# Optimization experiments

Hardware: AMD Instinct MI355X
Metric: run time of the kernel (lower is better)

The kernel has to match this reference:

```python
import jax, jax.numpy as jnp
import numpy as np

# Reconstructed from DAT's DAttentionBaseline with the wrapper's config:
# q_size=(14,14), n_heads=12, n_head_channels=64, n_groups=8, stride=1,
# offset_range_factor=1.0, use_pe=False (so log_cpb/rpe unused), no_off=False,
# ksize=3, dropout=0 (eval). Followed by the wrapper's Linear out-projection.

H = W = 14
G = 8          # n_groups
NH = 12        # n_heads
OFF_RANGE_FACTOR = 1.0


def grid_sample_bilinear(img, grid):
    # img: [B, C, H, W]; grid: [B, Hg, Wg, 2] in (x, y) order, [-1, 1],
    # align_corners=True, padding_mode='zeros' (torch defaults used by DAT).
    B, C, Hi, Wi = img.shape
    gx = (grid[..., 0] + 1.0) * 0.5 * (Wi - 1)
    gy = (grid[..., 1] + 1.0) * 0.5 * (Hi - 1)
    x0 = jnp.floor(gx)
    y0 = jnp.floor(gy)
    x1 = x0 + 1.0
    y1 = y0 + 1.0
    wx1 = gx - x0
    wx0 = 1.0 - wx1
    wy1 = gy - y0
    wy0 = 1.0 - wy1
    flat = img.reshape(B, C, Hi * Wi)

    def tap(xi, yi, wgt):
        valid = (xi >= 0) & (xi <= Wi - 1) & (yi >= 0) & (yi <= Hi - 1)
        xi_c = jnp.clip(xi, 0, Wi - 1).astype(jnp.int32)
        yi_c = jnp.clip(yi, 0, Hi - 1).astype(jnp.int32)
        idx = (yi_c * Wi + xi_c).reshape(B, 1, -1)
        vals = jnp.take_along_axis(flat, idx, axis=2)  # [B, C, Hg*Wg]
        w = (wgt * valid.astype(img.dtype)).reshape(B, 1, -1)
        return vals * w

    out = (tap(x0, y0, wx0 * wy0) + tap(x1, y0, wx1 * wy0)
           + tap(x0, y1, wx0 * wy1) + tap(x1, y1, wx1 * wy1))
    return out  # [B, C, Hg*Wg]


def setup_inputs() -> dict:
    key = jax.random.key(0)
    ks = jax.random.split(key, 16)
    B, N, C = 128, 196, 768
    Cg = C // G  # 96
    s = 0.02
    return {
        "hidden_states": jax.random.normal(ks[0], (B, N, C), jnp.float32),
        "Wq": jax.random.normal(ks[1], (C, C), jnp.float32) * s,
        "bq": jnp.zeros((C,), jnp.float32),
        "off_dw_w": jax.random.normal(ks[2], (Cg, 1, 3, 3), jnp.float32) * s,
        "off_dw_b": jnp.zeros((Cg,), jnp.float32),
        "ln_w": jnp.ones((Cg,), jnp.float32),
        "ln_b": jnp.zeros((Cg,), jnp.float32),
        "off_pw_w": jax.random.normal(ks[3], (2, Cg), jnp.float32) * s,
        "Wk": jax.random.normal(ks[4], (C, C), jnp.float32) * s,
        "bk": jnp.zeros((C,), jnp.float32),
        "Wv": jax.random.normal(ks[5], (C, C), jnp.float32) * s,
        "bv": jnp.zeros((C,), jnp.float32),
        "Wproj": jax.random.normal(ks[6], (C, C), jnp.float32) * s,
        "bproj": jnp.zeros((C,), jnp.float32),
        "Wout": jax.random.normal(ks[7], (C, C), jnp.float32) * s,
        "bout": jnp.zeros((C,), jnp.float32),
    }


def reference(hidden_states, Wq, bq, off_dw_w, off_dw_b, ln_w, ln_b, off_pw_w,
              Wk, bk, Wv, bv, Wproj, bproj, Wout, bout):
    B, N, C = hidden_states.shape
    Cg = C // G
    nh, dh = NH, C // NH
    scale = dh ** -0.5
    dt = hidden_states.dtype

    x_im = hidden_states.reshape(B, H, W, C).transpose(0, 3, 1, 2)  # [B,C,H,W]

    # proj_q: 1x1 conv
    q_im = jnp.einsum('bchw,oc->bohw', x_im, Wq) + bq[None, :, None, None]
    q_off = q_im.reshape(B * G, Cg, H, W)

    # offset net: depthwise 3x3 conv -> LayerNorm(channels) -> GELU -> 1x1 (no bias)
    t = jax.lax.conv_general_dilated(
        q_off, off_dw_w, (1, 1), [(1, 1), (1, 1)],
        dimension_numbers=('NCHW', 'OIHW', 'NCHW'), feature_group_count=Cg)
    t = t + off_dw_b[None, :, None, None]
    mu = t.mean(axis=1, keepdims=True)
    var = ((t - mu) ** 2).mean(axis=1, keepdims=True)
    t = (t - mu) * jax.lax.rsqrt(var + 1e-5)
    t = t * ln_w[None, :, None, None] + ln_b[None, :, None, None]
    t = jax.nn.gelu(t, approximate=False)
    off = jnp.einsum('bchw,oc->bohw', t, off_pw_w)  # [B*G, 2(y,x), H, W]

    off_range = jnp.array([1.0 / (H - 1), 1.0 / (W - 1)], dt).reshape(1, 2, 1, 1)
    off = jnp.tanh(off) * off_range * OFF_RANGE_FACTOR
    off = off.transpose(0, 2, 3, 1)  # [B*G, H, W, 2] (y, x)

    ry = ((jnp.arange(H, dtype=dt) + 0.5) / H) * 2.0 - 1.0
    rx = ((jnp.arange(W, dtype=dt) + 0.5) / W) * 2.0 - 1.0
    ref = jnp.stack(jnp.meshgrid(ry, rx, indexing='ij'), axis=-1)  # [H,W,2]
    pos = off + ref[None]          # (y, x)
    grid = pos[..., ::-1]          # (x, y) for grid_sample

    x_g = x_im.reshape(B * G, Cg, H, W)
    n_sample = H * W
    x_s = grid_sample_bilinear(x_g, grid).reshape(B, C, n_sample)

    k = jnp.einsum('bcn,oc->bon', x_s, Wk) + bk[None, :, None]
    v = jnp.einsum('bcn,oc->bon', x_s, Wv) + bv[None, :, None]

    qh = q_im.reshape(B, nh, dh, N)
    kh = k.reshape(B, nh, dh, n_sample)
    vh = v.reshape(B, nh, dh, n_sample)

    attn = jax.nn.softmax(jnp.einsum('bhcm,bhcn->bhmn', qh, kh) * scale, axis=-1)
    out = jnp.einsum('bhmn,bhcn->bhcm', attn, vh).reshape(B, C, N)

    y = jnp.einsum('bcn,oc->bon', out, Wproj) + bproj[None, :, None]
    y = y.transpose(0, 2, 1)               # [B, N, C]
    y = y @ Wout.T + bout                  # wrapper's Linear out-projection
    return y, attn
```

## Files before the change

kernel.cpp:

```cpp
#include <hip/hip_runtime.h>
#include <math.h>

#define Bsz 128
#define Hh 14
#define Ww 14
#define Nn 196
#define Cc 768
#define Gg 8
#define CgC 96
#define NHh 12
#define Dh 64
#define ROWS (Bsz*Nn)

typedef _Float16 half8 __attribute__((ext_vector_type(8)));
typedef _Float16 half4 __attribute__((ext_vector_type(4)));
typedef float f32x4 __attribute__((ext_vector_type(4)));

typedef __attribute__((address_space(3))) void LDSv;
typedef __attribute__((address_space(1))) void GLBv;

__global__ __launch_bounds__(256) void cvt_w5(
    const float* __restrict__ w0, const float* __restrict__ w1,
    const float* __restrict__ w2, const float* __restrict__ w3,
    const float* __restrict__ w4, _Float16* __restrict__ dst)
{
  const int i = blockIdx.x * 256 + threadIdx.x;
  const int per = Cc * Cc / 8;
  if (i >= 5 * per) return;
  const int m = i / per, r = i - m * per;
  const float* s = (m == 0) ? w0 : (m == 1) ? w1 : (m == 2) ? w2 : (m == 3) ? w3 : w4;
  float4 a = *(const float4*)(s + (size_t)r * 8);
  float4 b = *(const float4*)(s + (size_t)r * 8 + 4);
  half8 h;
  h[0]=(_Float16)a.x; h[1]=(_Float16)a.y; h[2]=(_Float16)a.z; h[3]=(_Float16)a.w;
  h[4]=(_Float16)b.x; h[5]=(_Float16)b.y; h[6]=(_Float16)b.z; h[7]=(_Float16)b.w;
  *(half8*)(dst + (size_t)m * Cc * Cc + (size_t)r * 8) = h;
}

__global__ __launch_bounds__(256) void fuse_bias(
    const float* __restrict__ Wo, const float* __restrict__ bp,
    const float* __restrict__ bo, float* __restrict__ bf)
{
  __shared__ float red[256];
  const int o2 = blockIdx.x;
  const int tid = threadIdx.x;
  const float* wrow = Wo + (size_t)o2 * Cc;
  float s = 0.f;
  for (int o = tid; o < Cc; o += 256) s = fmaf(wrow[o], bp[o], s);
  red[tid] = s;
  __syncthreads();
  for (int st = 128; st > 0; st >>= 1) { if (tid < st) red[tid] += red[tid + st]; __syncthreads(); }
  if (tid == 0) bf[o2] = red[0] + bo[o2];
}

__global__ __launch_bounds__(256) void gemm_ww(
    const _Float16* __restrict__ Wo16, const _Float16* __restrict__ Wp16,
    _Float16* __restrict__ Wf)
{
  __shared__ __align__(16) _Float16 As[128 * 64];
  __shared__ __align__(16) _Float16 Bs[128 * 72];
  const int t = threadIdx.x;
  const int bid = blockIdx.x;
  const int colb = bid % 6, rowb = bid / 6;
  const int row0 = rowb * 128, col0 = colb * 128;
  const int lane = t & 63, w = t >> 6;
  const int wr = w >> 1, wc = w & 1;
  const int l15 = lane & 15, l4 = lane >> 4;
  const int srow = t >> 3;
  const int sg   = t & 7;

  f32x4 acc[4][4];
#pragma unroll
  for (int i = 0; i < 4; ++i)
#pragma unroll
    for (int j = 0; j < 4; ++j) acc[i][j] = (f32x4){0.f, 0.f, 0.f, 0.f};

  for (int kt = 0; kt < 12; ++kt) {
    const int k0 = kt * 64;
#pragma unroll
    for (int it = 0; it < 4; ++it) {
      const int r = it * 32 + srow;
      half8 ha = *(const half8*)(Wo16 + (size_t)(row0 + r) * Cc + k0 + sg * 8);
      *(half8*)&As[r * 64 + ((sg ^ (r & 7)) * 8)] = ha;
    }
    {
      const int og = t >> 4;
      const int cg = t & 15;
#pragma unroll
      for (int it = 0; it < 4; ++it) {
        const int o = it * 16 + og;
        half8 hv = *(const half8*)(Wp16 + (size_t)(k0 + o) * Cc + col0 + cg * 8);
#pragma unroll
        for (int e = 0; e < 8; ++e)
          Bs[(cg * 8 + e) * 72 + o] = hv[e];
      }
    }
    __syncthreads();
#pragma unroll
    for (int ks = 0; ks < 2; ++ks) {
      half8 af[4], bf[4];
#pragma unroll
      for (int mi = 0; mi < 4; ++mi) {
        const int r = wr * 64 + mi * 16 + l15;
        const int g = ks * 4 + l4;
        af[mi] = *(const half8*)&As[r * 64 + ((g ^ (r & 7)) * 8)];
      }
#pragma unroll
      for (int ni = 0; ni < 4; ++ni) {
        const int c = wc * 64 + ni * 16 + l15;
        bf[ni] = *(const half8*)&Bs[c * 72 + ks * 32 + l4 * 8];
      }
#pragma unroll
      for (int mi = 0; mi < 4; ++mi)
#pragma unroll
        for (int ni = 0; ni < 4; ++ni)
          acc[mi][ni] = __builtin_amdgcn_mfma_f32_16x16x32_f16(af[mi], bf[ni], acc[mi][ni], 0, 0, 0);
    }
    __syncthreads();
  }

#pragma unroll
  for (int ni = 0; ni < 4; ++ni) {
    const int col = col0 + wc * 64 + ni * 16 + l15;
#pragma unroll
    for (int mi = 0; mi < 4; ++mi) {
      f32x4 v = acc[mi][ni];
      const int rbase = row0 + wr * 64 + mi * 16 + l4 * 4;
#pragma unroll
      for (int r = 0; r < 4; ++r)
        Wf[(size_t)(rbase + r) * Cc + col] = (_Float16)v[r];
    }
  }
}

__global__ __launch_bounds__(256) void gemm_f32a(
    const float* __restrict__ A, const _Float16* __restrict__ W,
    const float* __restrict__ bias, _Float16* __restrict__ Cout)
{
  __shared__ __align__(16) _Float16 As[128 * 64];
  __shared__ __align__(16) _Float16 Bs[128 * 64];
  const int t = threadIdx.x;
  const int nwg = gridDim.x;
  int bid = blockIdx.x;
  bid = (bid & 7) * (nwg >> 3) + (bid >> 3);
  const int colb = bid % 6, rowb = bid / 6;
  const int row0 = rowb * 128, col0 = colb * 128;
  const int lane = t & 63, w = t >> 6;
  const int wr = w >> 1, wc = w & 1;
  const int l15 = lane & 15, l4 = lane >> 4;
  const int srow = t >> 3;
  const int sg   = t & 7;
  const int rl = lane >> 3;
  const int sl = lane & 7;

  f32x4 acc[4][4];
#pragma unroll
  for (int i = 0; i < 4; ++i)
#pragma unroll
    for (int j = 0; j < 4; ++j) acc[i][j] = (f32x4){0.f, 0.f, 0.f, 0.f};

  for (int kt = 0; kt < 12; ++kt) {
    const int k0 = kt * 64;
#pragma unroll
    for (int it = 0; it < 4; ++it) {
      const int rbase = it * 32 + w * 8;
      const int rw = rbase + rl;
      const int sa = sl ^ (rw & 7);
      __builtin_amdgcn_global_load_lds(
          (GLBv*)(W + (size_t)(col0 + rw) * Cc + k0 + sa * 8),
          (LDSv*)&Bs[rbase * 64], 16, 0, 0);
      const int r = it * 32 + srow;
      const float* ap = A + (size_t)(row0 + r) * Cc + k0 + sg * 8;
      float4 a0 = *(const float4*)ap;
      float4 a1 = *(const float4*)(ap + 4);
      half8 ha;
      ha[0]=(_Float16)a0.x; ha[1]=(_Float16)a0.y; ha[2]=(_Float16)a0.z; ha[3]=(_Float16)a0.w;
      ha[4]=(_Float16)a1.x; ha[5]=(_Float16)a1.y; ha[6]=(_Float16)a1.z; ha[7]=(_Float16)a1.w;
      *(half8*)&As[r * 64 + ((sg ^ (r & 7)) * 8)] = ha;
    }
    __syncthreads();
#pragma unroll
    for (int ks = 0; ks < 2; ++ks) {
      half8 af[4], bf[4];
#pragma unroll
      for (int mi = 0; mi < 4; ++mi) {
        const int r = wr * 64 + mi * 16 + l15;
        const int g = ks * 4 + l4;
        af[mi] = *(const half8*)&As[r * 64 + ((g ^ (r & 7)) * 8)];
      }
#pragma unroll
      for (int ni = 0; ni < 4; ++ni) {
        const int r = wc * 64 + ni * 16 + l15;
        const int g = ks * 4 + l4;
        bf[ni] = *(const half8*)&Bs[r * 64 + ((g ^ (r & 7)) * 8)];
      }
#pragma unroll
      for (int mi = 0; mi < 4; ++mi)
#pragma unroll
        for (int ni = 0; ni < 4; ++ni)
          acc[mi][ni] = __builtin_amdgcn_mfma_f32_16x16x32_f16(af[mi], bf[ni], acc[mi][ni], 0, 0, 0);
    }
    __syncthreads();
  }

#pragma unroll
  for (int ni = 0; ni < 4; ++ni) {
    const int col = col0 + wc * 64 + ni * 16 + l15;
    const float bcol = bias[col];
#pragma unroll
    for (int mi = 0; mi < 4; ++mi) {
      f32x4 v = acc[mi][ni];
      const int rbase = row0 + wr * 64 + mi * 16 + l4 * 4;
#pragma unroll
      for (int r = 0; r < 4; ++r)
        Cout[(size_t)(rbase + r) * Cc + col] = (_Float16)(v[r] + bcol);
    }
  }
}

template<int F16OUT>
__global__ __launch_bounds__(256) void gemm_h16(
    const _Float16* __restrict__ A, const _Float16* __restrict__ W,
    const float* __restrict__ bias, void* __restrict__ Cout)
{
  __shared__ __align__(16) _Float16 As[128 * 64];
  __shared__ __align__(16) _Float16 Bs[128 * 64];
  const int t = threadIdx.x;
  const int nwg = gridDim.x;
  int bid = blockIdx.x;
  bid = (bid & 7) * (nwg >> 3) + (bid >> 3);
  const int colb = bid % 6, rowb = bid / 6;
  const int row0 = rowb * 128, col0 = colb * 128;
  const int lane = t & 63, w = t >> 6;
  const int wr = w >> 1, wc = w & 1;
  const int l15 = lane & 15, l4 = lane >> 4;
  const int rl = lane >> 3;
  const int sl = lane & 7;

  f32x4 acc[4][4];
#pragma unroll
  for (int i = 0; i < 4; ++i)
#pragma unroll
    for (int j = 0; j < 4; ++j) acc[i][j] = (f32x4){0.f, 0.f, 0.f, 0.f};

  for (int kt = 0; kt < 12; ++kt) {
    const int k0 = kt * 64;
#pragma unroll
    for (int it = 0; it < 4; ++it) {
      const int rbase = it * 32 + w * 8;
      const int r = rbase + rl;
      const int sa = sl ^ (r & 7);
      __builtin_amdgcn_global_load_lds(
          (GLBv*)(A + (size_t)(row0 + r) * Cc + k0 + sa * 8),
          (LDSv*)&As[rbase * 64], 16, 0, 0);
      __builtin_amdgcn_global_load_lds(
          (GLBv*)(W + (size_t)(col0 + r) * Cc + k0 + sa * 8),
          (LDSv*)&Bs[rbase * 64], 16, 0, 0);
    }
    __syncthreads();
#pragma unroll
    for (int ks = 0; ks < 2; ++ks) {
      half8 af[4], bf[4];
#pragma unroll
      for (int mi = 0; mi < 4; ++mi) {
        const int r = wr * 64 + mi * 16 + l15;
        const int g = ks * 4 + l4;
        af[mi] = *(const half8*)&As[r * 64 + ((g ^ (r & 7)) * 8)];
      }
#pragma unroll
      for (int ni = 0; ni < 4; ++ni) {
        const int r = wc * 64 + ni * 16 + l15;
        const int g = ks * 4 + l4;
        bf[ni] = *(const half8*)&Bs[r * 64 + ((g ^ (r & 7)) * 8)];
      }
#pragma unroll
      for (int mi = 0; mi < 4; ++mi)
#pragma unroll
        for (int ni = 0; ni < 4; ++ni)
          acc[mi][ni] = __builtin_amdgcn_mfma_f32_16x16x32_f16(af[mi], bf[ni], acc[mi][ni], 0, 0, 0);
    }
    __syncthreads();
  }

#pragma unroll
  for (int ni = 0; ni < 4; ++ni) {
    const int col = col0 + wc * 64 + ni * 16 + l15;
    const float bcol = bias[col];
#pragma unroll
    for (int mi = 0; mi < 4; ++mi) {
      f32x4 v = acc[mi][ni];
      const int rbase = row0 + wr * 64 + mi * 16 + l4 * 4;
#pragma unroll
      for (int r = 0; r < 4; ++r) {
        if (F16OUT) {
          ((_Float16*)Cout)[(size_t)(rbase + r) * Cc + col] = (_Float16)(v[r] + bcol);
        } else {
          ((float*)Cout)[(size_t)(rbase + r) * Cc + col] = v[r] + bcol;
        }
      }
    }
  }
}

__global__ __launch_bounds__(256) void gemm_h16_kv(
    const _Float16* __restrict__ A, const _Float16* __restrict__ Wkv,
    const float* __restrict__ bk, const float* __restrict__ bv,
    _Float16* __restrict__ K16, _Float16* __restrict__ V16)
{
  __shared__ __align__(16) _Float16 As[128 * 64];
  __shared__ __align__(16) _Float16 Bs[128 * 64];
  const int t = threadIdx.x;
  const int nwg = gridDim.x;
  int bid = blockIdx.x;
  bid = (bid & 7) * (nwg >> 3) + (bid >> 3);
  const int colb = bid % 12, rowb = bid / 12;
  const int row0 = rowb * 128, col0 = colb * 128;
  const int lane = t & 63, w = t >> 6;
  const int wr = w >> 1, wc = w & 1;
  const int l15 = lane & 15, l4 = lane >> 4;
  const int rl = lane >> 3;
  const int sl = lane & 7;

  _Float16* Cout = (colb < 6) ? K16 : V16;
  const float* bias = (colb < 6) ? bk : bv;
  const int cadj = (colb < 6) ? 0 : Cc;

  f32x4 acc[4][4];
#pragma unroll
  for (int i = 0; i < 4; ++i)
#pragma unroll
    for (int j = 0; j < 4; ++j) acc[i][j] = (f32x4){0.f, 0.f, 0.f, 0.f};

  for (int kt = 0; kt < 12; ++kt) {
    const int k0 = kt * 64;
#pragma unroll
    for (int it = 0; it < 4; ++it) {
      const int rbase = it * 32 + w * 8;
      const int r = rbase + rl;
      const int sa = sl ^ (r & 7);
      __builtin_amdgcn_global_load_lds(
          (GLBv*)(A + (size_t)(row0 + r) * Cc + k0 + sa * 8),
          (LDSv*)&As[rbase * 64], 16, 0, 0);
      __builtin_amdgcn_global_load_lds(
          (GLBv*)(Wkv + (size_t)(col0 + r) * Cc + k0 + sa * 8),
          (LDSv*)&Bs[rbase * 64], 16, 0, 0);
    }
    __syncthreads();
#pragma unroll
    for (int ks = 0; ks < 2; ++ks) {
      half8 af[4], bf[4];
#pragma unroll
      for (int mi = 0; mi < 4; ++mi) {
        const int r = wr * 64 + mi * 16 + l15;
        const int g = ks * 4 + l4;
        af[mi] = *(const half8*)&As[r * 64 + ((g ^ (r & 7)) * 8)];
      }
#pragma unroll
      for (int ni = 0; ni < 4; ++ni) {
        const int r = wc * 64 + ni * 16 + l15;
        const int g = ks * 4 + l4;
        bf[ni] = *(const half8*)&Bs[r * 64 + ((g ^ (r & 7)) * 8)];
      }
#pragma unroll
      for (int mi = 0; mi < 4; ++mi)
#pragma unroll
        for (int ni = 0; ni < 4; ++ni)
          acc[mi][ni] = __builtin_amdgcn_mfma_f32_16x16x32_f16(af[mi], bf[ni], acc[mi][ni], 0, 0, 0);
    }
    __syncthreads();
  }

#pragma unroll
  for (int ni = 0; ni < 4; ++ni) {
    const int col = col0 + wc * 64 + ni * 16 + l15;
    const float bcol = bias[col - cadj];
#pragma unroll
    for (int mi = 0; mi < 4; ++mi) {
      f32x4 v = acc[mi][ni];
      const int rbase = row0 + wr * 64 + mi * 16 + l4 * 4;
#pragma unroll
      for (int r = 0; r < 4; ++r)
        Cout[(size_t)(rbase + r) * Cc + (col - cadj)] = (_Float16)(v[r] + bcol);
    }
  }
}

__global__ __launch_bounds__(512, 4) void offset_sample(
    const _Float16* __restrict__ Q16, const float* __restrict__ hidden,
    const float* __restrict__ dw_w, const float* __restrict__ dw_b,
    const float* __restrict__ ln_w, const float* __restrict__ ln_b,
    const float* __restrict__ pw_w, _Float16* __restrict__ XS)
{
  __shared__ float Qs[8 * Ww * CgC];
  const int tid = threadIdx.x;
  const int g    = blockIdx.x & 7;
  const int half = blockIdx.x >> 3;
  const int b = blockIdx.y;
  const int cl = tid & 31;
  const int grp = tid >> 5;
  const int hbase = half ? 6 : 0;

  const size_t base = (size_t)b * Nn * Cc + g * CgC;
  for (int i = tid; i < 8 * Ww * 12; i += 512) {
    const int n = i / 12, j = i - n * 12;
    const int gn = hbase * Ww + n;
    half8 hv = *(const half8*)(Q16 + base + (size_t)gn * Cc + j * 8);
#pragma unroll
    for (int e = 0; e < 8; ++e) Qs[n * CgC + j * 8 + e] = (float)hv[e];
  }

  float wdw[3][9], bdw[3], wln[3], bln[3], wp0[3], wp1[3];
#pragma unroll
  for (int k = 0; k < 3; ++k) {
    const int c = cl + k * 32;
#pragma unroll
    for (int t9 = 0; t9 < 9; ++t9) wdw[k][t9] = dw_w[c * 9 + t9];
    bdw[k] = dw_b[c];
    wln[k] = ln_w[c];
    bln[k] = ln_b[c];
    wp0[k] = pw_w[c];
    wp1[k] = pw_w[CgC + c];
  }
  __syncthreads();

  const float* hb0 = hidden + base;
  const int nsites = 7 * Ww;

  for (int s0 = 0; s0 < nsites; s0 += 16) {
    const int slcl = s0 + grp;
    if (slcl < nsites) {
      const int site = half * nsites + slcl;
      const int h = site / Ww, w = site % Ww;

      float t[3];
#pragma unroll
      for (int k = 0; k < 3; ++k) t[k] = bdw[k];
#pragma unroll
      for (int ky = 0; ky < 3; ++ky) {
        const int hp = h + ky - 1;
        if (hp < 0 || hp > Hh - 1) continue;
#pragma unroll
        for (int kx = 0; kx < 3; ++kx) {
          const int wp = w + kx - 1;
          if (wp < 0 || wp > Ww - 1) continue;
          const float* row = &Qs[((hp - hbase) * Ww + wp) * CgC + cl];
#pragma unroll
          for (int k = 0; k < 3; ++k)
            t[k] = fmaf(row[k * 32], wdw[k][ky * 3 + kx], t[k]);
        }
      }

      float s = t[0] + t[1] + t[2];
#pragma unroll
      for (int off = 1; off <= 16; off <<= 1) s += __shfl_xor(s, off, 32);
      const float mu = s * (1.f / 96.f);
      float d2 = 0.f;
#pragma unroll
      for (int k = 0; k < 3; ++k) { const float d = t[k] - mu; d2 = fmaf(d, d, d2); }
#pragma unroll
      for (int off = 1; off <= 16; off <<= 1) d2 += __shfl_xor(d2, off, 32);
      const float rstd = rsqrtf(d2 * (1.f / 96.f) + 1e-5f);

      float p0 = 0.f, p1 = 0.f;
#pragma unroll
      for (int k = 0; k < 3; ++k) {
        const float tn = (t[k] - mu) * rstd * wln[k] + bln[k];
        const float a = 0.5f * tn * (1.f + erff(tn * 0.70710678118654752f));
        p0 = fmaf(a, wp0[k], p0);
        p1 = fmaf(a, wp1[k], p1);
      }
#pragma unroll
      for (int off = 1; off <= 16; off <<= 1) {
        p0 += __shfl_xor(p0, off, 32);
        p1 += __shfl_xor(p1, off, 32);
      }

      const float offy = tanhf(p0) * (1.f / 13.f);
      const float offx = tanhf(p1) * (1.f / 13.f);
      const float refy = (h + 0.5f) / 14.f * 2.f - 1.f;
      const float refx = (w + 0.5f) / 14.f * 2.f - 1.f;
      const float gx = ((offx + refx) + 1.f) * 0.5f * 13.f;
      const float gy = ((offy + refy) + 1.f) * 0.5f * 13.f;

      const float x0f = floorf(gx), y0f = floorf(gy);
      const int x0 = (int)x0f, y0 = (int)y0f;
      const float wx1 = gx - x0f, wx0 = 1.f - wx1;
      const float wy1 = gy - y0f, wy0 = 1.f - wy1;
      const bool vx0 = (x0 >= 0) & (x0 <= 13), vx1 = (x0 + 1 >= 0) & (x0 + 1 <= 13);
      const bool vy0 = (y0 >= 0) & (y0 <= 13), vy1 = (y0 + 1 >= 0) & (y0 + 1 <= 13);
      float acc[3] = {0.f, 0.f, 0.f};
#pragma unroll
      for (int k = 0; k < 3; ++k) {
        const int c = cl + k * 32;
        if (vx0 & vy0) acc[k] = fmaf(wx0 * wy0, hb0[(size_t)(y0 * Ww + x0) * Cc + c], acc[k]);
        if (vx1 & vy0) acc[k] = fmaf(wx1 * wy0, hb0[(size_t)(y0 * Ww + x0 + 1) * Cc + c], acc[k]);
        if (vx0 & vy1) acc[k] = fmaf(wx0 * wy1, hb0[(size_t)((y0 + 1) * Ww + x0) * Cc + c], acc[k]);
        if (vx1 & vy1) acc[k] = fmaf(wx1 * wy1, hb0[(size_t)((y0 + 1) * Ww + x0 + 1) * Cc + c], acc[k]);
      }
      _Float16* xp = XS + ((size_t)b * Nn + site) * Cc + g * CgC + cl;
#pragma unroll
      for (int k = 0; k < 3; ++k) xp[k * 32] = (_Float16)acc[k];
    }
  }
}

__global__ __launch_bounds__(512, 4) void attn_fused(
    const _Float16* __restrict__ Qm, const _Float16* __restrict__ Km,
    const _Float16* __restrict__ Vm, float* __restrict__ attn,
    _Float16* __restrict__ OUT)
{
  __shared__ __align__(16) _Float16 Kt[208 * 72];
  __shared__ __align__(16) _Float16 Vt[64 * 232];
  __shared__ __align__(16) _Float16 Ps[8][16 * 40];
  const int tid = threadIdx.x;
  const int hh = blockIdx.x, b = blockIdx.y;
  const int lane = tid & 63, wv = tid >> 6;
  const int l15 = lane & 15, l4 = lane >> 4;

  const _Float16* Qbase = Qm + (size_t)b * Nn * Cc + hh * Dh;
  const _Float16* Kbase = Km + (size_t)b * Nn * Cc + hh * Dh;
  const _Float16* Vbase = Vm + (size_t)b * Nn * Cc + hh * Dh;

  {
    const int g = tid & 7;
    for (int n = tid >> 3; n < 208; n += 64) {
      half8 hv = {};
      if (n < Nn) hv = *(const half8*)(Kbase + (size_t)n * Cc + g * 8);
      *(half8*)&Kt[n * 72 + g * 8] = hv;
    }
  }
  {
    const int d0 = (tid & 15) * 4;
    for (int n = tid >> 4; n < Nn; n += 32) {
      half4 v = *(const half4*)(Vbase + (size_t)n * Cc + d0);
      Vt[(d0 + 0) * 232 + n] = v[0];
      Vt[(d0 + 1) * 232 + n] = v[1];
      Vt[(d0 + 2) * 232 + n] = v[2];
      Vt[(d0 + 3) * 232 + n] = v[3];
    }
    for (int e = tid; e < 64 * 36; e += 512) {
      int d = e / 36, n = Nn + e % 36;
      Vt[d * 232 + n] = (_Float16)0.f;
    }
  }
  __syncthreads();

  for (int mt = wv; mt < 13; mt += 8) {
    const int qrow = mt * 16 + l15;
    const _Float16* qp = Qbase + (size_t)(qrow < Nn ? qrow : (Nn - 1)) * Cc + l4 * 8;
    half8 aq0 = *(const half8*)qp;
    half8 aq1 = *(const half8*)(qp + 32);

    f32x4 accs[13];
#pragma unroll
    for (int nt = 0; nt < 13; ++nt) accs[nt] = (f32x4){0.f, 0.f, 0.f, 0.f};
    __builtin_amdgcn_s_setprio(1);
#pragma unroll
    for (int nt = 0; nt < 13; ++nt) {
      const int rb = (nt * 16 + l15) * 72;
      half8 bk0 = *(const half8*)&Kt[rb + l4 * 8];
      half8 bk1 = *(const half8*)&Kt[rb + 32 + l4 * 8];
      accs[nt] = __builtin_amdgcn_mfma_f32_16x16x32_f16(aq0, bk0, accs[nt], 0, 0, 0);
      accs[nt] = __builtin_amdgcn_mfma_f32_16x16x32_f16(aq1, bk1, accs[nt], 0, 0, 0);
    }
    __builtin_amdgcn_s_setprio(0);

    float rmax[4] = {-1e30f, -1e30f, -1e30f, -1e30f};
#pragma unroll
    for (int nt = 0; nt < 13; ++nt) {
#pragma unroll
      for (int r = 0; r < 4; ++r) {
        float s = accs[nt][r] * 0.125f;
        if (nt == 12 && l15 >= 4) s = -1e30f;
        accs[nt][r] = s;
        rmax[r] = fmaxf(rmax[r], s);
      }
    }
#pragma unroll
    for (int off = 1; off <= 8; off <<= 1)
#pragma unroll
      for (int r = 0; r < 4; ++r)
        rmax[r] = fmaxf(rmax[r], __shfl_xor(rmax[r], off, 64));

    float rsum[4] = {0.f, 0.f, 0.f, 0.f};
#pragma unroll
    for (int nt = 0; nt < 13; ++nt) {
#pragma unroll
      for (int r = 0; r < 4; ++r) {
        float p = __expf(accs[nt][r] - rmax[r]);
        accs[nt][r] = p;
        rsum[r] += p;
      }
    }
#pragma unroll
    for (int off = 1; off <= 8; off <<= 1)
#pragma unroll
      for (int r = 0; r < 4; ++r)
        rsum[r] += __shfl_xor(rsum[r], off, 64);
    float rinv[4];
#pragma unroll
    for (int r = 0; r < 4; ++r) rinv[r] = 1.f / rsum[r];

    float* ab = attn + (((size_t)b * NHh + hh) * Nn) * (size_t)Nn;
#pragma unroll
    for (int nt = 0; nt < 13; ++nt) {
      const int n = nt * 16 + l15;
#pragma unroll
      for (int r = 0; r < 4; ++r) {
        float pr = accs[nt][r] * rinv[r];
        accs[nt][r] = pr;
        const int m = mt * 16 + l4 * 4 + r;
        if (m < Nn && n < Nn) ab[(size_t)m * Nn + n] = pr;
      }
    }

    f32x4 acco[4];
#pragma unroll
    for (int dt = 0; dt < 4; ++dt) acco[dt] = (f32x4){0.f, 0.f, 0.f, 0.f};
#pragma unroll
    for (int nsl = 0; nsl < 7; ++nsl) {
#pragma unroll
      for (int h2 = 0; h2 < 2; ++h2) {
        const int nt = nsl * 2 + h2;
        if (nt < 13) {
#pragma unroll
          for (int r = 0; r < 4; ++r)
            Ps[wv][(l4 * 4 + r) * 40 + h2 * 16 + l15] = (_Float16)accs[nt][r];
        } else {
#pragma unroll
          for (int r = 0; r < 4; ++r)
            Ps[wv][(l4 * 4 + r) * 40 + h2 * 16 + l15] = (_Float16)0.f;
        }
      }
      half8 ap = *(const half8*)&Ps[wv][l15 * 40 + l4 * 8];
      __builtin_amdgcn_s_setprio(1);
#pragma unroll
      for (int dt = 0; dt < 4; ++dt) {
        half8 bv = *(const half8*)&Vt[(dt * 16 + l15) * 232 + nsl * 32 + l4 * 8];
        acco[dt] = __builtin_amdgcn_mfma_f32_16x16x32_f16(ap, bv, acco[dt], 0, 0, 0);
      }
      __builtin_amdgcn_s_setprio(0);
    }
#pragma unroll
    for (int dt = 0; dt < 4; ++dt) {
#pragma unroll
      for (int r = 0; r < 4; ++r) {
        const int m = mt * 16 + l4 * 4 + r;
        if (m < Nn)
          OUT[((size_t)b * Nn + m) * Cc + hh * Dh + dt * 16 + l15] = (_Float16)acco[dt][r];
      }
    }
  }
}

extern "C" void kernel_launch(void* const* d_in, const int* in_sizes, int n_in,
                              void* d_out, int out_size, void* d_ws, size_t ws_size,
                              hipStream_t stream) {
  const float* hidden = (const float*)d_in[0];
  const float* Wq = (const float*)d_in[1];
  const float* bq = (const float*)d_in[2];
  const float* dw_w = (const float*)d_in[3];
  const float* dw_b = (const float*)d_in[4];
  const float* ln_w = (const float*)d_in[5];
  const float* ln_b = (const float*)d_in[6];
  const float* pw_w = (const float*)d_in[7];
  const float* Wk = (const float*)d_in[8];
  const float* bk = (const float*)d_in[9];
  const float* Wv = (const float*)d_in[10];
  const float* bv = (const float*)d_in[11];
  const float* Wp = (const float*)d_in[12];
  const float* bp = (const float*)d_in[13];
  const float* Wo = (const float*)d_in[14];
  const float* bo = (const float*)d_in[15];

  const size_t SZ = (size_t)Bsz * Nn * Cc;
  float* yout = (float*)d_out;
  float* attn = yout + SZ;

  _Float16* Q16   = (_Float16*)d_ws;
  _Float16* XS16  = Q16   + SZ;
  _Float16* K16   = XS16  + SZ;
  _Float16* V16   = K16   + SZ;
  _Float16* OUT16 = V16   + SZ;
  _Float16* W16   = OUT16 + SZ;
  _Float16* Wf16  = W16   + 5 * (size_t)Cc * Cc;
  float*    bf    = (float*)(Wf16 + (size_t)Cc * Cc);

  const int gemm_blocks = (ROWS / 128) * (Cc / 128);
  const int kv_blocks   = (ROWS / 128) * 12;

  cvt_w5<<<(5 * Cc * Cc / 8 + 255) / 256, 256, 0, stream>>>(Wq, Wk, Wv, Wp, Wo, W16);
  gemm_ww<<<36, 256, 0, stream>>>(W16 + 4 * (size_t)Cc * Cc, W16 + 3 * (size_t)Cc * Cc, Wf16);
  fuse_bias<<<Cc, 256, 0, stream>>>(Wo, bp, bo, bf);

  gemm_f32a<<<gemm_blocks, 256, 0, stream>>>(hidden, W16 + 0 * (size_t)Cc * Cc, bq, Q16);
  offset_sample<<<dim3(Gg * 2, Bsz), 512, 0, stream>>>(Q16, hidden, dw_w, dw_b, ln_w, ln_b, pw_w, XS16);
  gemm_h16_kv<<<kv_blocks, 256, 0, stream>>>(XS16, W16 + 1 * (size_t)Cc * Cc, bk, bv, K16, V16);
  attn_fused<<<dim3(NHh, Bsz), 512, 0, stream>>>(Q16, K16, V16, attn, OUT16);
  gemm_h16<0><<<gemm_blocks, 256, 0, stream>>>(OUT16, Wf16, bf, yout);
}
```

Before: 495.2 us.

## Write V transposed from KV GEMM, recompute QK scores with online softmax stats

The KV GEMM epilogue now writes V directly in a per-batch, per-channel transposed layout padded to 224 columns. A new kernel zeroes that padding. The attention kernel reads V straight from global memory instead of staging a transpose in LDS, and shrinks the K tile stride. Softmax is restructured into a streaming first pass that only tracks row max and sum, followed by recomputing QK scores while writing probabilities, so the 13 score tiles no longer sit in registers. Occupancy is raised to 6 blocks. In exchange the QK MFMAs run twice, V loads come uncached from global memory inside the inner loop, and the transposed V stores are scattered.

```diff
diff --git a/kernel.cpp b/kernel.cpp
--- a/kernel.cpp
+++ b/kernel.cpp
@@ -11,6 +11,7 @@
 #define NHh 12
 #define Dh 64
 #define ROWS (Bsz*Nn)
+#define VNS 224
 
 typedef _Float16 half8 __attribute__((ext_vector_type(8)));
 typedef _Float16 half4 __attribute__((ext_vector_type(4)));
@@ -35,6 +36,15 @@
   h[0]=(_Float16)a.x; h[1]=(_Float16)a.y; h[2]=(_Float16)a.z; h[3]=(_Float16)a.w;
   h[4]=(_Float16)b.x; h[5]=(_Float16)b.y; h[6]=(_Float16)b.z; h[7]=(_Float16)b.w;
   *(half8*)(dst + (size_t)m * Cc * Cc + (size_t)r * 8) = h;
+}
+
+__global__ __launch_bounds__(256) void zero_vpad(_Float16* __restrict__ Vt)
+{
+  const int i = blockIdx.x * 256 + threadIdx.x;
+  const int total = Bsz * Cc * 28 / 4;
+  if (i >= total) return;
+  const int row = i / 7, j = (i - row * 7) * 4;
+  *(half4*)(Vt + (size_t)row * VNS + 196 + j) = (half4){(_Float16)0.f,(_Float16)0.f,(_Float16)0.f,(_Float16)0.f};
 }
 
 __global__ __launch_bounds__(256) void fuse_bias(
@@ -305,7 +315,7 @@
 __global__ __launch_bounds__(256) void gemm_h16_kv(
     const _Float16* __restrict__ A, const _Float16* __restrict__ Wkv,
     const float* __restrict__ bk, const float* __restrict__ bv,
-    _Float16* __restrict__ K16, _Float16* __restrict__ V16)
+    _Float16* __restrict__ K16, _Float16* __restrict__ V16t)
 {
   __shared__ __align__(16) _Float16 As[128 * 64];
   __shared__ __align__(16) _Float16 Bs[128 * 64];
@@ -321,10 +331,6 @@
   const int rl = lane >> 3;
   const int sl = lane & 7;
 
-  _Float16* Cout = (colb < 6) ? K16 : V16;
-  const float* bias = (colb < 6) ? bk : bv;
-  const int cadj = (colb < 6) ? 0 : Cc;
-
   f32x4 acc[4][4];
 #pragma unroll
   for (int i = 0; i < 4; ++i)
@@ -370,17 +376,36 @@
     __syncthreads();
   }
 
-#pragma unroll
-  for (int ni = 0; ni < 4; ++ni) {
-    const int col = col0 + wc * 64 + ni * 16 + l15;
-    const float bcol = bias[col - cadj];
-#pragma unroll
-    for (int mi = 0; mi < 4; ++mi) {
-      f32x4 v = acc[mi][ni];
-      const int rbase = row0 + wr * 64 + mi * 16 + l4 * 4;
-#pragma unroll
-      for (int r = 0; r < 4; ++r)
-        Cout[(size_t)(rbase + r) * Cc + (col - cadj)] = (_Float16)(v[r] + bcol);
+  if (colb < 6) {
+#pragma unroll
+    for (int ni = 0; ni < 4; ++ni) {
+      const int col = col0 + wc * 64 + ni * 16 + l15;
+      const float bcol = bk[col];
+#pragma unroll
+      for (int mi = 0; mi < 4; ++mi) {
+        f32x4 v = acc[mi][ni];
+        const int rbase = row0 + wr * 64 + mi * 16 + l4 * 4;
+#pragma unroll
+        for (int r = 0; r < 4; ++r)
+          K16[(size_t)(rbase + r) * Cc + col] = (_Float16)(v[r] + bcol);
+      }
+    }
+  } else {
+#pragma unroll
+    for (int ni = 0; ni < 4; ++ni) {
+      const int dg = col0 - Cc + wc * 64 + ni * 16 + l15;
+      const float bcol = bv[dg];
+#pragma unroll
+      for (int mi = 0; mi < 4; ++mi) {
+        f32x4 v = acc[mi][ni];
+        const int rbase = row0 + wr * 64 + mi * 16 + l4 * 4;
+#pragma unroll
+        for (int r = 0; r < 4; ++r) {
+          const int rt = rbase + r;
+          const int bb = rt / Nn, nn = rt - bb * Nn;
+          V16t[((size_t)bb * Cc + dg) * VNS + nn] = (_Float16)(v[r] + bcol);
+        }
+      }
     }
   }
 }
@@ -504,13 +529,12 @@
   }
 }
 
-__global__ __launch_bounds__(512, 4) void attn_fused(
+__global__ __launch_bounds__(512, 6) void attn_fused(
     const _Float16* __restrict__ Qm, const _Float16* __restrict__ Km,
-    const _Float16* __restrict__ Vm, float* __restrict__ attn,
+    const _Float16* __restrict__ Vtg, float* __restrict__ attn,
     _Float16* __restrict__ OUT)
 {
-  __shared__ __align__(16) _Float16 Kt[208 * 72];
-  __shared__ __align__(16) _Float16 Vt[64 * 232];
+  __shared__ __align__(16) _Float16 Kt[208 * 68];
   __shared__ __align__(16) _Float16 Ps[8][16 * 40];
   const int tid = threadIdx.x;
   const int hh = blockIdx.x, b = blockIdx.y;
@@ -519,28 +543,14 @@
 
   const _Float16* Qbase = Qm + (size_t)b * Nn * Cc + hh * Dh;
   const _Float16* Kbase = Km + (size_t)b * Nn * Cc + hh * Dh;
-  const _Float16* Vbase = Vm + (size_t)b * Nn * Cc + hh * Dh;
+  const _Float16* Vg = Vtg + ((size_t)b * Cc + hh * Dh) * VNS;
 
   {
     const int g = tid & 7;
     for (int n = tid >> 3; n < 208; n += 64) {
       half8 hv = {};
       if (n < Nn) hv = *(const half8*)(Kbase + (size_t)n * Cc + g * 8);
-      *(half8*)&Kt[n * 72 + g * 8] = hv;
-    }
-  }
-  {
-    const int d0 = (tid & 15) * 4;
-    for (int n = tid >> 4; n < Nn; n += 32) {
-      half4 v = *(const half4*)(Vbase + (size_t)n * Cc + d0);
-      Vt[(d0 + 0) * 232 + n] = v[0];
-      Vt[(d0 + 1) * 232 + n] = v[1];
-      Vt[(d0 + 2) * 232 + n] = v[2];
-      Vt[(d0 + 3) * 232 + n] = v[3];
-    }
-    for (int e = tid; e < 64 * 36; e += 512) {
-      int d = e / 36, n = Nn + e % 36;
-      Vt[d * 232 + n] = (_Float16)0.f;
+      *(half8*)&Kt[n * 68 + g * 8] = hv;
     }
   }
   __syncthreads();
@@ -551,68 +561,44 @@
     half8 aq0 = *(const half8*)qp;
     half8 aq1 = *(const half8*)(qp + 32);
 
-    f32x4 accs[13];
-#pragma unroll
-    for (int nt = 0; nt < 13; ++nt) accs[nt] = (f32x4){0.f, 0.f, 0.f, 0.f};
-    __builtin_amdgcn_s_setprio(1);
-#pragma unroll
+    float m_pl[4] = {-1e30f, -1e30f, -1e30f, -1e30f};
+    float l_pl[4] = {0.f, 0.f, 0.f, 0.f};
     for (int nt = 0; nt < 13; ++nt) {
-      const int rb = (nt * 16 + l15) * 72;
+      f32x4 acc = (f32x4){0.f, 0.f, 0.f, 0.f};
+      const int rb = (nt * 16 + l15) * 68;
       half8 bk0 = *(const half8*)&Kt[rb + l4 * 8];
       half8 bk1 = *(const half8*)&Kt[rb + 32 + l4 * 8];
-      accs[nt] = __builtin_amdgcn_mfma_f32_16x16x32_f16(aq0, bk0, accs[nt], 0, 0, 0);
-      accs[nt] = __builtin_amdgcn_mfma_f32_16x16x32_f16(aq1, bk1, accs[nt], 0, 0, 0);
-    }
-    __builtin_amdgcn_s_setprio(0);
-
-    float rmax[4] = {-1e30f, -1e30f, -1e30f, -1e30f};
-#pragma unroll
-    for (int nt = 0; nt < 13; ++nt) {
+      acc = __builtin_amdgcn_mfma_f32_16x16x32_f16(aq0, bk0, acc, 0, 0, 0);
+      acc = __builtin_amdgcn_mfma_f32_16x16x32_f16(aq1, bk1, acc, 0, 0, 0);
+      const bool masked = (nt == 12) && (l15 >= 4);
 #pragma unroll
       for (int r = 0; r < 4; ++r) {
-        float s = accs[nt][r] * 0.125f;
-        if (nt == 12 && l15 >= 4) s = -1e30f;
-        accs[nt][r] = s;
-        rmax[r] = fmaxf(rmax[r], s);
-      }
-    }
+        float s = masked ? -1e30f : acc[r] * 0.125f;
+        const float mn = fmaxf(m_pl[r], s);
+        l_pl[r] = l_pl[r] * __expf(m_pl[r] - mn) + __expf(s - mn);
+        m_pl[r] = mn;
+      }
+    }
+    float m_row[4], l_row[4];
+#pragma unroll
+    for (int r = 0; r < 4; ++r) m_row[r] = m_pl[r];
 #pragma unroll
     for (int off = 1; off <= 8; off <<= 1)
 #pragma unroll
       for (int r = 0; r < 4; ++r)
-        rmax[r] = fmaxf(rmax[r], __shfl_xor(rmax[r], off, 64));
-
-    float rsum[4] = {0.f, 0.f, 0.f, 0.f};
-#pragma unroll
-    for (int nt = 0; nt < 13; ++nt) {
-#pragma unroll
-      for (int r = 0; r < 4; ++r) {
-        float p = __expf(accs[nt][r] - rmax[r]);
-        accs[nt][r] = p;
-        rsum[r] += p;
-      }
-    }
+        m_row[r] = fmaxf(m_row[r], __shfl_xor(m_row[r], off, 64));
+#pragma unroll
+    for (int r = 0; r < 4; ++r) l_row[r] = l_pl[r] * __expf(m_pl[r] - m_row[r]);
 #pragma unroll
     for (int off = 1; off <= 8; off <<= 1)
 #pragma unroll
       for (int r = 0; r < 4; ++r)
-        rsum[r] += __shfl_xor(rsum[r], off, 64);
+        l_row[r] += __shfl_xor(l_row[r], off, 64);
     float rinv[4];
 #pragma unroll
-    for (int r = 0; r < 4; ++r) rinv[r] = 1.f / rsum[r];
+    for (int r = 0; r < 4; ++r) rinv[r] = 1.f / l_row[r];
 
     float* ab = attn + (((size_t)b * NHh + hh) * Nn) * (size_t)Nn;
-#pragma unroll
-    for (int nt = 0; nt < 13; ++nt) {
-      const int n = nt * 16 + l15;
-#pragma unroll
-      for (int r = 0; r < 4; ++r) {
-        float pr = accs[nt][r] * rinv[r];
-        accs[nt][r] = pr;
-        const int m = mt * 16 + l4 * 4 + r;
-        if (m < Nn && n < Nn) ab[(size_t)m * Nn + n] = pr;
-      }
-    }
 
     f32x4 acco[4];
 #pragma unroll
@@ -623,9 +609,21 @@
       for (int h2 = 0; h2 < 2; ++h2) {
         const int nt = nsl * 2 + h2;
         if (nt < 13) {
-#pragma unroll
-          for (int r = 0; r < 4; ++r)
-            Ps[wv][(l4 * 4 + r) * 40 + h2 * 16 + l15] = (_Float16)accs[nt][r];
+          f32x4 acc = (f32x4){0.f, 0.f, 0.f, 0.f};
+          const int rb = (nt * 16 + l15) * 68;
+          half8 bk0 = *(const half8*)&Kt[rb + l4 * 8];
+          half8 bk1 = *(const half8*)&Kt[rb + 32 + l4 * 8];
+          acc = __builtin_amdgcn_mfma_f32_16x16x32_f16(aq0, bk0, acc, 0, 0, 0);
+          acc = __builtin_amdgcn_mfma_f32_16x16x32_f16(aq1, bk1, acc, 0, 0, 0);
+          const bool masked = (nt == 12) && (l15 >= 4);
+          const int n = nt * 16 + l15;
+#pragma unroll
+          for (int r = 0; r < 4; ++r) {
+            float p = masked ? 0.f : __expf(acc[r] * 0.125f - m_row[r]) * rinv[r];
+            Ps[wv][(l4 * 4 + r) * 40 + h2 * 16 + l15] = (_Float16)p;
+            const int m = mt * 16 + l4 * 4 + r;
+            if (m < Nn && n < Nn) ab[(size_t)m * Nn + n] = p;
+          }
         } else {
 #pragma unroll
           for (int r = 0; r < 4; ++r)
@@ -636,7 +634,7 @@
       __builtin_amdgcn_s_setprio(1);
 #pragma unroll
       for (int dt = 0; dt < 4; ++dt) {
-        half8 bv = *(const half8*)&Vt[(dt * 16 + l15) * 232 + nsl * 32 + l4 * 8];
+        half8 bv = *(const half8*)(Vg + (size_t)(dt * 16 + l15) * VNS + nsl * 32 + l4 * 8);
         acco[dt] = __builtin_amdgcn_mfma_f32_16x16x32_f16(ap, bv, acco[dt], 0, 0, 0);
       }
       __builtin_amdgcn_s_setprio(0);
@@ -674,14 +672,15 @@
   const float* bo = (const float*)d_in[15];
 
   const size_t SZ = (size_t)Bsz * Nn * Cc;
+  const size_t SZV = (size_t)Bsz * Cc * VNS;
   float* yout = (float*)d_out;
   float* attn = yout + SZ;
 
   _Float16* Q16   = (_Float16*)d_ws;
   _Float16* XS16  = Q16   + SZ;
   _Float16* K16   = XS16  + SZ;
-  _Float16* V16   = K16   + SZ;
-  _Float16* OUT16 = V16   + SZ;
+  _Float16* V16t  = K16   + SZ;
+  _Float16* OUT16 = V16t  + SZV;
   _Float16* W16   = OUT16 + SZ;
   _Float16* Wf16  = W16   + 5 * (size_t)Cc * Cc;
   float*    bf    = (float*)(Wf16 + (size_t)Cc * Cc);
@@ -690,12 +689,13 @@
   const int kv_blocks   = (ROWS / 128) * 12;
 
   cvt_w5<<<(5 * Cc * Cc / 8 + 255) / 256, 256, 0, stream>>>(Wq, Wk, Wv, Wp, Wo, W16);
+  zero_vpad<<<(Bsz * Cc * 28 / 4 + 255) / 256, 256, 0, stream>>>(V16t);
   gemm_ww<<<36, 256, 0, stream>>>(W16 + 4 * (size_t)Cc * Cc, W16 + 3 * (size_t)Cc * Cc, Wf16);
   fuse_bias<<<Cc, 256, 0, stream>>>(Wo, bp, bo, bf);
 
   gemm_f32a<<<gemm_blocks, 256, 0, stream>>>(hidden, W16 + 0 * (size_t)Cc * Cc, bq, Q16);
   offset_sample<<<dim3(Gg * 2, Bsz), 512, 0, stream>>>(Q16, hidden, dw_w, dw_b, ln_w, ln_b, pw_w, XS16);
-  gemm_h16_kv<<<kv_blocks, 256, 0, stream>>>(XS16, W16 + 1 * (size_t)Cc * Cc, bk, bv, K16, V16);
-  attn_fused<<<dim3(NHh, Bsz), 512, 0, stream>>>(Q16, K16, V16, attn, OUT16);
+  gemm_h16_kv<<<kv_blocks, 256, 0, stream>>>(XS16, W16 + 1 * (size_t)Cc * Cc, bk, bv, K16, V16t);
+  attn_fused<<<dim3(NHh, Bsz), 512, 0, stream>>>(Q16, K16, V16t, attn, OUT16);
   gemm_h16<0><<<gemm_blocks, 256, 0, stream>>>(OUT16, Wf16, bf, yout);
 }
```

Result: slower. 765.4 us (+54.6%).
